# Performance work log

Measured on AMD Instinct MI355X. Metric: run time of the kernel, lower is better.

## Reference

```python
import jax, jax.numpy as jnp
import numpy as np

NUM_BFS_ROUNDS = 32      # fixed-iteration replacement for the set-based BFS (enough hops for N=4096, k=20)
VORONOI_CHUNK = 1024     # must divide B*N


def _knn_self(points, K):
    # brute-force self-KNN over [B,N,3]; idx[...,0] is the query point itself
    sq = jnp.sum(points * points, -1)
    dist = sq[:, :, None] + sq[:, None, :] - 2.0 * jnp.einsum('bnd,bmd->bnm', points, points)
    N = points.shape[1]
    dist = jnp.where(jnp.eye(N, dtype=bool)[None], -1.0, dist)  # force self to rank first
    _, idx = jax.lax.top_k(-dist, K)
    return idx  # [B,N,K] int32


def _gather(x, idx):
    # x [B,N,D], idx [B,N,K] -> [B,N,K,D]
    return jax.vmap(lambda xb, ib: xb[ib])(x, idx)


def _disambiguate(normals, idx):
    # BFS normal-orientation propagation from point 0 (frontier shared across batch, as in the torch code)
    B, N, _ = normals.shape
    frontier0 = jnp.zeros((N,), bool).at[0].set(True)
    visited0 = jnp.zeros((N,), bool)

    def step(carry, _):
        nrm, visited, frontier = carry
        safe_idx = jnp.where(frontier[None, :, None], idx, N)  # non-frontier rows scatter to dummy slot N
        cur = _gather(nrm, idx)                                 # [B,N,K,3]
        sign = jnp.where(jnp.sum(cur * cur[:, :, 0:1, :], -1, keepdims=True) > 0, 1.0, -1.0)
        renew = cur * sign

        def scat(nb, ib, rb):
            pad = jnp.concatenate([nb, jnp.zeros((1, 3), nb.dtype)], 0)
            return pad.at[ib.reshape(-1)].set(rb.reshape(-1, 3))[:N]

        nrm = jax.vmap(scat)(nrm, safe_idx, renew)
        mark = jnp.zeros((N + 1,), bool).at[safe_idx[:, :, 1:].reshape(-1)].set(True)[:N]
        visited = visited | frontier
        frontier = mark & ~visited
        return (nrm, visited, frontier), None

    (normals, _, _), _ = jax.lax.scan(step, (normals, visited0, frontier0), None, length=NUM_BFS_ROUNDS)
    return normals


def _frames_field(points, idx):
    knn_pts = _gather(points, idx)                              # [B,N,K,3]
    centered = knn_pts - knn_pts.mean(-2, keepdims=True)
    # NOTE: divides by (last_dim - 1) == 2, faithfully replicating the original code
    cov = jnp.einsum('bnki,bnkj->bnij', centered, centered) / 2.0
    _, vecs = jnp.linalg.eigh(cov)                              # ascending eigenvalues
    frames = jnp.swapaxes(vecs, -1, -2)                         # rows = eigenvectors; row 0 = normal
    frames = frames.at[:, :, 0, :].set(_disambiguate(frames[:, :, 0, :], idx))
    det = jnp.linalg.det(frames)
    frames = frames.at[:, :, 1, :].set(frames[:, :, 1, :] * det[..., None])
    return frames, knn_pts


def _forward(points, k, local_W):
    B, N = points.shape[:2]
    idx = _knn_self(points, k)
    frames, knn_pts = _frames_field(points, idx)
    dpt = knn_pts - points[:, :, None, :]                       # [B,N,K,3]
    t1 = frames[:, :, 1, :]
    t2 = frames[:, :, 2, :]
    dpt_t = jnp.stack([jnp.sum(dpt * t1[:, :, None, :], -1),
                       jnp.sum(dpt * t2[:, :, None, :], -1)], -1)   # [B,N,K,2]

    # ---- local voronoi area on tangent-plane grid ----
    bmin = dpt_t.min(-2) * 1.1                                  # [B,N,2]
    bmax = dpt_t.max(-2) * 1.1
    maxlen = (bmax - bmin).max(-1)                              # [B,N]
    coord = (dpt_t - bmin[:, :, None, :]) / maxlen[:, :, None, None] * 2.0 - 1.0
    lin = jnp.linspace(-1.0, 1.0, local_W, dtype=points.dtype)
    X, Y = jnp.meshgrid(lin, lin, indexing='ij')
    grid = jnp.stack([X, Y], -1).reshape(-1, 2)                 # [W^2, 2]
    coords_c = jax.lax.stop_gradient(coord).reshape(-1, VORONOI_CHUNK, k, 2)

    def chunk_count(c):  # c [C,k,2] -> count of grid cells whose nearest local point is the center (idx 0)
        d = jnp.sum((grid[None, :, None, :] - c[:, None, :, :]) ** 2, -1)  # [C,W^2,k]
        return jnp.sum(jnp.argmin(d, -1) == 0, -1)

    counts = jax.lax.map(chunk_count, coords_c).reshape(B, N).astype(points.dtype)
    area = counts * maxlen ** 2 / float((local_W - 1) ** 2)     # [B,N]

    # ---- Weingarten fields (non-strict branch) -> gaussian curvature ----
    normals = frames[:, :, 0, :]
    dnrm = _gather(normals, idx) - normals[:, :, None, :]
    dnrm_t = jnp.stack([jnp.sum(dnrm * t1[:, :, None, :], -1),
                        jnp.sum(dnrm * t2[:, :, None, :], -1)], -1)  # [B,N,K,2]
    XXT = jnp.einsum('bnki,bnkj->bnij', dpt_t, dpt_t)
    YXT = jnp.einsum('bnki,bnkj->bnij', dnrm_t, dpt_t)
    Wmat = YXT @ jnp.linalg.inv(XXT + 1e-8 * jnp.eye(2, dtype=points.dtype))
    Wmat = (Wmat + jnp.swapaxes(Wmat, -1, -2)) / 2.0
    gauss = jnp.linalg.det(Wmat)                                # [B,N]

    euler = jnp.sum(gauss * area, -1) / np.pi / 2.0             # [B]
    return euler


def setup_inputs() -> dict:
    key = jax.random.key(0)
    pointscloud = jax.random.normal(key, (2, 4096, 3), dtype=jnp.float32)
    return {"pointscloud": pointscloud, "k": 20, "local_W": 64}


def reference(pointscloud, k, local_W):
    return _forward(pointscloud, k, local_W)
```

## Files before the change

### kernel.cpp

```cpp
#include <hip/hip_runtime.h>
#include <math.h>

#define NPTS  4096
#define BATCH 2
#define KNB   20
#define WGRID 64
#define GCELLS (WGRID * WGRID)
#define NROUNDS 32
#define KBUF  192
#define KQ    16
#define NEDGE (BATCH * NPTS * KNB)
#define NPACK (NEDGE / 16)

__device__ __forceinline__ float knn_dist(const float4 c, const float px,
                                          const float py, const float pz,
                                          const float sqn, const int m,
                                          const int n) {
    const float dot = px * c.x + py * c.y + pz * c.z;
    float dist = (sqn + c.w) - 2.0f * dot;
    if (m == n) dist = -1.0f;
    return dist;
}

__device__ __forceinline__ unsigned long long knn_key(const float dist, const int m) {
    unsigned u = __float_as_uint(dist);
    u = (dist < 0.0f) ? ~u : (u | 0x80000000u);
    return ((unsigned long long)u << 32) | (unsigned)m;
}

__global__ __launch_bounds__(1024, 8) void knn_kernel(const float* __restrict__ pts,
                                                      int* __restrict__ idx) {
    const int tid  = threadIdx.x;
    const int lane = tid & 63;
    const int wid  = tid >> 6;
    const int q    = blockIdx.x * KQ + wid;
    const int b    = q >> 12;
    const int n    = q & (NPTS - 1);
    const float* P = pts + (size_t)b * NPTS * 3;

    __shared__ float4 spts[NPTS];
    __shared__ unsigned short buf[KQ][KBUF];

    for (int i = tid; i < NPTS; i += 1024) {
        const float x = P[i * 3 + 0], y = P[i * 3 + 1], z = P[i * 3 + 2];
        spts[i] = make_float4(x, y, z, x * x + y * y + z * z);
    }
    __syncthreads();

    const float4 me = spts[n];
    const float px = me.x, py = me.y, pz = me.z, sqn = me.w;

    float lmin = 3e38f;
#pragma unroll
    for (int step = 0; step < 64; ++step) {
        const int m = lane + step * 64;
        lmin = fminf(lmin, knn_dist(spts[m], px, py, pz, sqn, m, n));
    }

    float v = lmin;
#pragma unroll
    for (int k = 2; k <= 64; k <<= 1) {
#pragma unroll
        for (int j = k >> 1; j >= 1; j >>= 1) {
            const float o = __shfl_xor(v, j, 64);
            const bool up    = ((lane & k) == 0);
            const bool lower = ((lane & j) == 0);
            v = (lower == up) ? fminf(v, o) : fmaxf(v, o);
        }
    }
    float thr = __shfl(v, 19, 64);
    thr = thr + fabsf(thr) * 1e-4f + 1e-6f;

    unsigned short* wbuf = buf[wid];
    int cnt = 0;
#pragma unroll
    for (int step = 0; step < 64; ++step) {
        const int m = lane + step * 64;
        const float dist = knn_dist(spts[m], px, py, pz, sqn, m, n);
        const bool keep = (dist <= thr);
        const unsigned long long mask = __ballot(keep);
        if (keep) {
            const int pos = cnt + __popcll(mask & ((1ull << lane) - 1ull));
            if (pos < KBUF) wbuf[pos] = (unsigned short)m;
        }
        cnt += __popcll(mask);
    }

    const int M = (cnt < KBUF) ? cnt : KBUF;
    int* op = idx + (size_t)q * KNB;
    const unsigned long long MAXK = ~0ull;
    if (M <= 64) {
        unsigned long long key = MAXK;
        if (lane < M) {
            const int m = (int)wbuf[lane];
            key = knn_key(knn_dist(spts[m], px, py, pz, sqn, m, n), m);
        }
#pragma unroll
        for (int k = 2; k <= 64; k <<= 1) {
#pragma unroll
            for (int j = k >> 1; j >= 1; j >>= 1) {
                const unsigned long long o = __shfl_xor(key, j, 64);
                const bool up    = ((lane & k) == 0);
                const bool lower = ((lane & j) == 0);
                const bool takeMin = (lower == up);
                const unsigned long long mn = key < o ? key : o;
                const unsigned long long mx = key < o ? o : key;
                key = takeMin ? mn : mx;
            }
        }
        if (lane < KNB) op[lane] = (int)(unsigned)(key & 0xffffffffu);
    } else {
        unsigned long long s0 = MAXK, s1 = MAXK, s2 = MAXK;
        if (lane < M) {
            const int m = (int)wbuf[lane];
            s0 = knn_key(knn_dist(spts[m], px, py, pz, sqn, m, n), m);
        }
        if (lane + 64 < M) {
            const int m = (int)wbuf[lane + 64];
            s1 = knn_key(knn_dist(spts[m], px, py, pz, sqn, m, n), m);
        }
        if (lane + 128 < M) {
            const int m = (int)wbuf[lane + 128];
            s2 = knn_key(knn_dist(spts[m], px, py, pz, sqn, m, n), m);
        }
#pragma unroll 1
        for (int r = 0; r < KNB; ++r) {
            unsigned long long kk = s0 < s1 ? s0 : s1;
            kk = kk < s2 ? kk : s2;
#pragma unroll
            for (int off = 32; off; off >>= 1) {
                const unsigned long long ok = __shfl_xor(kk, off, 64);
                kk = ok < kk ? ok : kk;
            }
            if (s0 == kk) s0 = MAXK;
            else if (s1 == kk) s1 = MAXK;
            else if (s2 == kk) s2 = MAXK;
            if (lane == 0) op[r] = (int)(unsigned)(kk & 0xffffffffu);
        }
    }
}

template <int p, int q, int r>
__device__ __forceinline__ void jrot(double A[3][3], double V[3][3]) {
    double apq = A[p][q];
    if (fabs(apq) < 1e-300) return;
    double app = A[p][p], aqq = A[q][q];
    double tau = (aqq - app) / (2.0 * apq);
    double sq  = sqrt(1.0 + tau * tau);
    double t   = (tau >= 0.0) ? (1.0 / (tau + sq)) : (1.0 / (tau - sq));
    double c   = 1.0 / sqrt(1.0 + t * t);
    double s   = t * c;
    A[p][p] = app - t * apq; A[q][q] = aqq + t * apq;
    A[p][q] = 0.0; A[q][p] = 0.0;
    double arp = A[r][p], arq = A[r][q];
    A[r][p] = c * arp - s * arq; A[p][r] = A[r][p];
    A[r][q] = s * arp + c * arq; A[q][r] = A[r][q];
#pragma unroll
    for (int i = 0; i < 3; ++i) {
        double vip = V[i][p], viq = V[i][q];
        V[i][p] = c * vip - s * viq;
        V[i][q] = s * vip + c * viq;
    }
}

__device__ __forceinline__ double selV(const double V[3][3], int i, int c) {
    return c == 0 ? V[i][0] : (c == 1 ? V[i][1] : V[i][2]);
}

__global__ __launch_bounds__(64) void frames_kernel(const float* __restrict__ pts,
                                                    const int* __restrict__ idx,
                                                    float* __restrict__ frames,
                                                    float* __restrict__ normals) {
    const int g = blockIdx.x * 64 + threadIdx.x;
    const int b = g / NPTS;
    const float* P  = pts + (size_t)b * NPTS * 3;
    const int*   ip = idx + (size_t)g * KNB;

    float mx = 0.f, my = 0.f, mz = 0.f;
#pragma unroll
    for (int k = 0; k < KNB; ++k) {
        const int j = ip[k];
        mx += P[j * 3 + 0]; my += P[j * 3 + 1]; mz += P[j * 3 + 2];
    }
    mx /= 20.0f; my /= 20.0f; mz /= 20.0f;

    float c00 = 0.f, c01 = 0.f, c02 = 0.f, c11 = 0.f, c12 = 0.f, c22 = 0.f;
#pragma unroll
    for (int k = 0; k < KNB; ++k) {
        const int j = ip[k];
        const float x = P[j * 3 + 0] - mx;
        const float y = P[j * 3 + 1] - my;
        const float z = P[j * 3 + 2] - mz;
        c00 += x * x; c01 += x * y; c02 += x * z;
        c11 += y * y; c12 += y * z; c22 += z * z;
    }
    c00 *= 0.5f; c01 *= 0.5f; c02 *= 0.5f; c11 *= 0.5f; c12 *= 0.5f; c22 *= 0.5f;

    double A[3][3] = {{c00, c01, c02}, {c01, c11, c12}, {c02, c12, c22}};
    double V[3][3] = {{1, 0, 0}, {0, 1, 0}, {0, 0, 1}};
#pragma unroll
    for (int sw = 0; sw < 10; ++sw) {
        jrot<0, 1, 2>(A, V);
        jrot<0, 2, 1>(A, V);
        jrot<1, 2, 0>(A, V);
    }
    double e0 = A[0][0], e1 = A[1][1], e2 = A[2][2];
    int o0 = 0, o1 = 1, o2 = 2;
    if (e0 > e1) { double t = e0; e0 = e1; e1 = t; int o = o0; o0 = o1; o1 = o; }
    if (e1 > e2) { double t = e1; e1 = e2; e2 = t; int o = o1; o1 = o2; o2 = o; }
    if (e0 > e1) { double t = e0; e0 = e1; e1 = t; int o = o0; o0 = o1; o1 = o; }

    float* F = frames + (size_t)g * 9;
    F[0] = (float)selV(V, 0, o0); F[1] = (float)selV(V, 1, o0); F[2] = (float)selV(V, 2, o0);
    F[3] = (float)selV(V, 0, o1); F[4] = (float)selV(V, 1, o1); F[5] = (float)selV(V, 2, o1);
    F[6] = (float)selV(V, 0, o2); F[7] = (float)selV(V, 1, o2); F[8] = (float)selV(V, 2, o2);
    normals[(size_t)g * 3 + 0] = F[0];
    normals[(size_t)g * 3 + 1] = F[1];
    normals[(size_t)g * 3 + 2] = F[2];
}

__global__ __launch_bounds__(256) void edgesign_kernel(const int* __restrict__ idx,
                                                       const float* __restrict__ normals,
                                                       unsigned* __restrict__ dsgnp,
                                                       unsigned short* __restrict__ idx16) {
    const int e = blockIdx.x * 256 + threadIdx.x;
    const int lane = threadIdx.x & 63;
    const int b = e / (NPTS * KNB);
    const int r = e - b * NPTS * KNB;
    const int n = r / KNB;
    const int j = idx[e];
    idx16[e] = (unsigned short)j;
    const float* NB = normals + (size_t)b * NPTS * 3;
    const float d = __fadd_rn(__fadd_rn(__fmul_rn(NB[j * 3 + 0], NB[n * 3 + 0]),
                                        __fmul_rn(NB[j * 3 + 1], NB[n * 3 + 1])),
                              __fmul_rn(NB[j * 3 + 2], NB[n * 3 + 2]));
    const unsigned long long m0 = __ballot(d == 0.0f);
    const unsigned long long m1 = __ballot(d > 0.0f);
    if (lane < 4) {
        unsigned x = (unsigned)(m0 >> (lane * 16)) & 0xFFFFu;
        unsigned y = (unsigned)(m1 >> (lane * 16)) & 0xFFFFu;
        x = (x | (x << 8)) & 0x00FF00FFu; x = (x | (x << 4)) & 0x0F0F0F0Fu;
        x = (x | (x << 2)) & 0x33333333u; x = (x | (x << 1)) & 0x55555555u;
        y = (y | (y << 8)) & 0x00FF00FFu; y = (y | (y << 4)) & 0x0F0F0F0Fu;
        y = (y | (y << 2)) & 0x33333333u; y = (y | (y << 1)) & 0x55555555u;
        dsgnp[((e - lane) >> 4) + lane] = x | (y << 1);
    }
}

__global__ __launch_bounds__(1024) void bfs_kernel(const unsigned short* __restrict__ idx16,
                                                   const unsigned* __restrict__ dsgnp,
                                                   float* __restrict__ nrm) {
    const int tid = threadIdx.x;
    const int lane = tid & 63;
    __shared__ int winner[BATCH * NPTS];
    __shared__ signed char sgbuf[2][BATCH * NPTS];
    __shared__ unsigned dsp[NPACK];
    __shared__ unsigned short list[NPTS];
    __shared__ unsigned char EL[NPTS];
    __shared__ int cntsh;

    {
        unsigned wacc = 0;
        const uint4* ip4 = (const uint4*)idx16;
#pragma unroll 4
        for (int i = tid; i < (NEDGE * 2) / 16; i += 1024) {
            const uint4 v = ip4[i];
            wacc ^= v.x ^ v.y ^ v.z ^ v.w;
        }
        asm volatile("" :: "v"(wacc));
    }

    for (int j = tid; j < NPTS; j += 1024) {
        winner[j] = 0; winner[NPTS + j] = 0;
        sgbuf[0][j] = 1; sgbuf[0][NPTS + j] = 1;
        EL[j] = 0;
    }
    for (int i = tid; i < NPACK; i += 1024) dsp[i] = dsgnp[i];
    if (tid == 0) { cntsh = 1; list[0] = 0; EL[0] = 1; }
    __syncthreads();

    int cur = 0;
    int rstart = 0, rend = 1;
    for (int round = 0; round < NROUNDS; ++round) {
        const int tag = (round + 1) << 17;
        const int items = (rend - rstart) * BATCH;
        for (int base = 0; base < items; base += 4096) {
            unsigned pr[4][KNB / 2];
            int tflat[4], wbase[4];
            bool ok[4];
#pragma unroll
            for (int s = 0; s < 4; ++s) {
                const int w = base + s * 1024 + tid;
                ok[s] = (w < items);
                if (ok[s]) {
                    const int i = w >> 1, b = w & 1;
                    const int n0 = (int)list[rstart + i];
                    tflat[s] = tag + n0 * KNB;
                    wbase[s] = b * NPTS;
                    const unsigned* rp =
                        (const unsigned*)(idx16 + ((size_t)b * NPTS + n0) * KNB);
#pragma unroll
                    for (int u = 0; u < KNB / 2; ++u) pr[s][u] = rp[u];
                }
            }
#pragma unroll
            for (int s = 0; s < 4; ++s) {
                if (ok[s]) {
#pragma unroll
                    for (int u = 0; u < KNB / 2; ++u) {
                        const int j0 = (int)(pr[s][u] & 0xffffu);
                        const int j1 = (int)(pr[s][u] >> 16);
                        atomicMax(&winner[wbase[s] + j0], tflat[s] + 2 * u);
                        atomicMax(&winner[wbase[s] + j1], tflat[s] + 2 * u + 1);
                    }
                }
            }
        }
        __syncthreads();
        const signed char* sgOld = sgbuf[cur];
        signed char* sgNew = sgbuf[cur ^ 1];
#pragma unroll
        for (int u = 0; u < 4; ++u) {
            const int j = tid + u * 1024;
            bool marked = false;
#pragma unroll
            for (int b = 0; b < BATCH; ++b) {
                const int bj = b * NPTS + j;
                const int w = winner[bj];
                signed char s = sgOld[bj];
                if (w >= tag) {
                    const int flat = w - tag;
                    const int nsrc = flat / KNB;
                    const int wi = b * (NPTS * KNB) + flat;
                    const int d = (int)((dsp[wi >> 4] >> ((wi & 15) << 1)) & 3u) - 1;
                    const signed char sn = sgOld[b * NPTS + nsrc];
                    s = d ? (signed char)(d * sn) : (signed char)(-s);
                    if (flat % KNB != 0) marked = true;
                }
                sgNew[bj] = s;
            }
            const bool f = marked && !EL[j];
            if (f) EL[j] = 1;
            const unsigned long long mask = __ballot(f);
            if (mask) {
                const int lead = (int)(__ffsll((long long)mask) - 1);
                int basep = 0;
                if (lane == lead) basep = atomicAdd(&cntsh, (int)__popcll(mask));
                basep = __shfl(basep, lead, 64);
                if (f) list[basep + (int)__popcll(mask & ((1ull << lane) - 1ull))] =
                           (unsigned short)j;
            }
        }
        __syncthreads();
        cur ^= 1;
        rstart = rend;
        rend = cntsh;
        if (rstart == rend) break;
    }
    const signed char* sgF = sgbuf[cur];
    for (int i = tid; i < BATCH * NPTS * 3; i += 1024) {
        if (sgF[i / 3] < 0) nrm[i] = -nrm[i];
    }
}

__global__ __launch_bounds__(256) void geom_kernel(const float* __restrict__ pts,
                                                   const int* __restrict__ idx,
                                                   const float* __restrict__ frames,
                                                   const float* __restrict__ nrm,
                                                   double* __restrict__ pervals) {
    const int lane = threadIdx.x & 63;
    const int q = blockIdx.x * 4 + (threadIdx.x >> 6);
    const int b = q >> 12, n = q & (NPTS - 1);
    const float* P  = pts + (size_t)b * NPTS * 3;
    const float* NR = nrm + (size_t)b * NPTS * 3;
    const float* F  = frames + (size_t)q * 9;

    const float v0x = NR[n * 3 + 0], v0y = NR[n * 3 + 1], v0z = NR[n * 3 + 2];
    const float v1x = F[3], v1y = F[4], v1z = F[5];
    const float v2x = F[6], v2y = F[7], v2z = F[8];
    const float det = v0x * (v1y * v2z - v1z * v2y)
                    - v0y * (v1x * v2z - v1z * v2x)
                    + v0z * (v1x * v2y - v1y * v2x);
    const float t1x = v1x * det, t1y = v1y * det, t1z = v1z * det;
    const float t2x = v2x, t2y = v2y, t2z = v2z;

    const bool isk = lane < KNB;
    float ptx = 0.f, pty = 0.f, qtx = 0.f, qty = 0.f;
    if (isk) {
        const int j = idx[(size_t)q * KNB + lane];
        const float dx = P[j * 3 + 0] - P[n * 3 + 0];
        const float dy = P[j * 3 + 1] - P[n * 3 + 1];
        const float dz = P[j * 3 + 2] - P[n * 3 + 2];
        ptx = dx * t1x + dy * t1y + dz * t1z;
        pty = dx * t2x + dy * t2y + dz * t2z;
        const float ex = NR[j * 3 + 0] - v0x;
        const float ey = NR[j * 3 + 1] - v0y;
        const float ez = NR[j * 3 + 2] - v0z;
        qtx = ex * t1x + ey * t1y + ez * t1z;
        qty = ex * t2x + ey * t2y + ez * t2z;
    }

    float mnx = isk ? ptx :  3e38f, mny = isk ? pty :  3e38f;
    float mxx = isk ? ptx : -3e38f, mxy = isk ? pty : -3e38f;
#pragma unroll
    for (int off = 32; off; off >>= 1) {
        mnx = fminf(mnx, __shfl_xor(mnx, off, 64));
        mny = fminf(mny, __shfl_xor(mny, off, 64));
        mxx = fmaxf(mxx, __shfl_xor(mxx, off, 64));
        mxy = fmaxf(mxy, __shfl_xor(mxy, off, 64));
    }
    mnx *= 1.1f; mny *= 1.1f; mxx *= 1.1f; mxy *= 1.1f;
    const float ml = fmaxf(mxx - mnx, mxy - mny);

    const float cx = (ptx - mnx) / ml * 2.0f - 1.0f;
    const float cy = (pty - mny) / ml * 2.0f - 1.0f;
    const float c0x = __shfl(cx, 0, 64), c0y = __shfl(cy, 0, 64);

    const float ax = 2.0f * (cx - c0x);
    const float ay = 2.0f * (cy - c0y);
    const float bbk = cx * cx + cy * cy - (c0x * c0x + c0y * c0y);
    const float inva = (ay != 0.0f) ? (1.0f / ay) : 0.0f;

    const float gx = (float)(-1.0 + (2.0 * (double)lane) / 63.0);
    float lo = -3e38f, hi = 3e38f;
    bool feas = true;
#pragma unroll
    for (int k = 1; k < KNB; ++k) {
        const float axk = __shfl(ax, k, 64);
        const float ayk = __shfl(ay, k, 64);
        const float bk  = __shfl(bbk, k, 64);
        const float ik  = __shfl(inva, k, 64);
        const float rk  = bk - gx * axk;
        const float t   = rk * ik;
        if (ayk > 0.0f)      hi = fminf(hi, t);
        else if (ayk < 0.0f) lo = fmaxf(lo, t);
        else                 feas = feas && (rk >= 0.0f);
    }
    int cnt = 0;
    if (feas) {
        const float hif = fminf((hi + 1.0f) * 31.5f, 63.0f);
        const float lof = fmaxf((lo + 1.0f) * 31.5f, 0.0f);
        const int jhi = (int)floorf(hif);
        const int jlo = (int)ceilf(lof);
        cnt = jhi - jlo + 1;
        if (cnt < 0) cnt = 0;
    }
#pragma unroll
    for (int off = 32; off; off >>= 1) cnt += __shfl_xor(cnt, off, 64);
    const float area = (float)cnt * ml * ml / 3969.0f;

    double xx00 = 0, xx01 = 0, xx11 = 0, yx00 = 0, yx01 = 0, yx10 = 0, yx11 = 0;
    if (isk) {
        const double px = ptx, py = pty, qx2 = qtx, qy2 = qty;
        xx00 = px * px; xx01 = px * py; xx11 = py * py;
        yx00 = qx2 * px; yx01 = qx2 * py; yx10 = qy2 * px; yx11 = qy2 * py;
    }
#pragma unroll
    for (int off = 32; off; off >>= 1) {
        xx00 += __shfl_xor(xx00, off, 64);
        xx01 += __shfl_xor(xx01, off, 64);
        xx11 += __shfl_xor(xx11, off, 64);
        yx00 += __shfl_xor(yx00, off, 64);
        yx01 += __shfl_xor(yx01, off, 64);
        yx10 += __shfl_xor(yx10, off, 64);
        yx11 += __shfl_xor(yx11, off, 64);
    }
    if (lane == 0) {
        const double m00 = xx00 + 1e-8, m01 = xx01, m11 = xx11 + 1e-8;
        const double dm = m00 * m11 - m01 * m01;
        const double i00 = m11 / dm, i01 = -m01 / dm, i11 = m00 / dm;
        const double w00 = yx00 * i00 + yx01 * i01;
        const double w01 = yx00 * i01 + yx01 * i11;
        const double w10 = yx10 * i00 + yx11 * i01;
        const double w11 = yx10 * i01 + yx11 * i11;
        const double off2 = 0.5 * (w01 + w10);
        const double gauss = w00 * w11 - off2 * off2;
        pervals[q] = gauss * (double)area;
    }
}

__global__ __launch_bounds__(256) void reduce_kernel(const double* __restrict__ pervals,
                                                     float* __restrict__ out) {
    const int b = blockIdx.x, tid = threadIdx.x;
    __shared__ double sm[256];
    double s = 0.0;
    for (int i = tid; i < NPTS; i += 256) s += pervals[(size_t)b * NPTS + i];
    sm[tid] = s;
    __syncthreads();
    for (int st = 128; st > 0; st >>= 1) {
        if (tid < st) sm[tid] += sm[tid + st];
        __syncthreads();
    }
    if (tid == 0) out[b] = (float)(sm[0] / 3.14159265358979323846 / 2.0);
}

extern "C" void kernel_launch(void* const* d_in, const int* in_sizes, int n_in,
                              void* d_out, int out_size, void* d_ws, size_t ws_size,
                              hipStream_t stream) {
    (void)in_sizes; (void)n_in; (void)out_size; (void)ws_size;
    const float* pts = (const float*)d_in[0];
    char* ws = (char*)d_ws;

    size_t off = 0;
    double* pervals = (double*)(ws + off); off += (size_t)BATCH * NPTS * sizeof(double);
    int*    idx     = (int*)(ws + off);    off += (size_t)BATCH * NPTS * KNB * sizeof(int);
    float*  frames  = (float*)(ws + off);  off += (size_t)BATCH * NPTS * 9 * sizeof(float);
    float*  normals = (float*)(ws + off);  off += (size_t)BATCH * NPTS * 3 * sizeof(float);
    unsigned short* idx16 = (unsigned short*)(ws + off);
    off += (size_t)BATCH * NPTS * KNB * sizeof(unsigned short);
    unsigned* dsgnp = (unsigned*)(ws + off);
    off += (size_t)NPACK * sizeof(unsigned);

    knn_kernel<<<BATCH * NPTS / KQ, 1024, 0, stream>>>(pts, idx);
    frames_kernel<<<BATCH * NPTS / 64, 64, 0, stream>>>(pts, idx, frames, normals);
    edgesign_kernel<<<BATCH * NPTS * KNB / 256, 256, 0, stream>>>(idx, normals, dsgnp, idx16);
    bfs_kernel<<<1, 1024, 0, stream>>>(idx16, dsgnp, normals);
    geom_kernel<<<BATCH * NPTS / 4, 256, 0, stream>>>(pts, idx, frames, normals, pervals);
    reduce_kernel<<<BATCH, 256, 0, stream>>>(pervals, (float*)d_out);
}
```

Before: 100.5 us.

## Process four KNN queries per wavefront to reuse shared point loads

Each wavefront in the KNN kernel now handles four query points instead of one. Every candidate float4 read from shared memory is reused across all four distance computations, and the bitonic threshold and sort steps are interleaved across queries. Blocks shrink to 512 threads with 32 queries each, so fewer blocks each stage the point cloud into LDS. The change also drops a prefetch/warm-up read of idx16 at the start of the BFS kernel. In exchange, register pressure rises and occupancy may fall.

```diff
diff --git a/kernel.cpp b/kernel.cpp
--- a/kernel.cpp
+++ b/kernel.cpp
@@ -8,7 +8,9 @@
 #define GCELLS (WGRID * WGRID)
 #define NROUNDS 32
 #define KBUF  192
-#define KQ    16
+#define KQW   4
+#define WPB   8
+#define QPB   (KQW * WPB)
 #define NEDGE (BATCH * NPTS * KNB)
 #define NPACK (NEDGE / 16)
 
@@ -28,114 +30,150 @@
     return ((unsigned long long)u << 32) | (unsigned)m;
 }
 
-__global__ __launch_bounds__(1024, 8) void knn_kernel(const float* __restrict__ pts,
-                                                      int* __restrict__ idx) {
+__global__ __launch_bounds__(512, 4) void knn_kernel(const float* __restrict__ pts,
+                                                     int* __restrict__ idx) {
     const int tid  = threadIdx.x;
     const int lane = tid & 63;
     const int wid  = tid >> 6;
-    const int q    = blockIdx.x * KQ + wid;
-    const int b    = q >> 12;
-    const int n    = q & (NPTS - 1);
+    const int qbase = blockIdx.x * QPB + wid * KQW;
+    const int b    = qbase >> 12;
     const float* P = pts + (size_t)b * NPTS * 3;
 
     __shared__ float4 spts[NPTS];
-    __shared__ unsigned short buf[KQ][KBUF];
-
-    for (int i = tid; i < NPTS; i += 1024) {
+    __shared__ unsigned short buf[QPB][KBUF];
+
+    for (int i = tid; i < NPTS; i += 512) {
         const float x = P[i * 3 + 0], y = P[i * 3 + 1], z = P[i * 3 + 2];
         spts[i] = make_float4(x, y, z, x * x + y * y + z * z);
     }
     __syncthreads();
 
-    const float4 me = spts[n];
-    const float px = me.x, py = me.y, pz = me.z, sqn = me.w;
-
-    float lmin = 3e38f;
-#pragma unroll
+    int nq[KQW];
+    float px[KQW], py[KQW], pz[KQW], sqn[KQW];
+#pragma unroll
+    for (int qq = 0; qq < KQW; ++qq) {
+        nq[qq] = (qbase & (NPTS - 1)) + qq;
+        const float4 me = spts[nq[qq]];
+        px[qq] = me.x; py[qq] = me.y; pz[qq] = me.z; sqn[qq] = me.w;
+    }
+
+    float v[KQW];
+#pragma unroll
+    for (int qq = 0; qq < KQW; ++qq) v[qq] = 3e38f;
+#pragma unroll 4
     for (int step = 0; step < 64; ++step) {
         const int m = lane + step * 64;
-        lmin = fminf(lmin, knn_dist(spts[m], px, py, pz, sqn, m, n));
-    }
-
-    float v = lmin;
+        const float4 c = spts[m];
+#pragma unroll
+        for (int qq = 0; qq < KQW; ++qq)
+            v[qq] = fminf(v[qq], knn_dist(c, px[qq], py[qq], pz[qq], sqn[qq], m, nq[qq]));
+    }
+
 #pragma unroll
     for (int k = 2; k <= 64; k <<= 1) {
 #pragma unroll
         for (int j = k >> 1; j >= 1; j >>= 1) {
-            const float o = __shfl_xor(v, j, 64);
             const bool up    = ((lane & k) == 0);
             const bool lower = ((lane & j) == 0);
-            v = (lower == up) ? fminf(v, o) : fmaxf(v, o);
-        }
-    }
-    float thr = __shfl(v, 19, 64);
-    thr = thr + fabsf(thr) * 1e-4f + 1e-6f;
-
-    unsigned short* wbuf = buf[wid];
-    int cnt = 0;
-#pragma unroll
+            const bool takeMin = (lower == up);
+#pragma unroll
+            for (int qq = 0; qq < KQW; ++qq) {
+                const float o = __shfl_xor(v[qq], j, 64);
+                v[qq] = takeMin ? fminf(v[qq], o) : fmaxf(v[qq], o);
+            }
+        }
+    }
+    float thr[KQW];
+#pragma unroll
+    for (int qq = 0; qq < KQW; ++qq) {
+        float t = __shfl(v[qq], 19, 64);
+        thr[qq] = t + fabsf(t) * 1e-4f + 1e-6f;
+    }
+
+    int cnt[KQW];
+#pragma unroll
+    for (int qq = 0; qq < KQW; ++qq) cnt[qq] = 0;
+#pragma unroll 2
     for (int step = 0; step < 64; ++step) {
         const int m = lane + step * 64;
-        const float dist = knn_dist(spts[m], px, py, pz, sqn, m, n);
-        const bool keep = (dist <= thr);
-        const unsigned long long mask = __ballot(keep);
-        if (keep) {
-            const int pos = cnt + __popcll(mask & ((1ull << lane) - 1ull));
-            if (pos < KBUF) wbuf[pos] = (unsigned short)m;
-        }
-        cnt += __popcll(mask);
-    }
-
-    const int M = (cnt < KBUF) ? cnt : KBUF;
-    int* op = idx + (size_t)q * KNB;
+        const float4 c = spts[m];
+#pragma unroll
+        for (int qq = 0; qq < KQW; ++qq) {
+            const float dist = knn_dist(c, px[qq], py[qq], pz[qq], sqn[qq], m, nq[qq]);
+            const bool keep = (dist <= thr[qq]);
+            const unsigned long long mask = __ballot(keep);
+            if (keep) {
+                const int pos = cnt[qq] + __popcll(mask & ((1ull << lane) - 1ull));
+                if (pos < KBUF) buf[wid * KQW + qq][pos] = (unsigned short)m;
+            }
+            cnt[qq] += __popcll(mask);
+        }
+    }
+
     const unsigned long long MAXK = ~0ull;
-    if (M <= 64) {
-        unsigned long long key = MAXK;
-        if (lane < M) {
-            const int m = (int)wbuf[lane];
-            key = knn_key(knn_dist(spts[m], px, py, pz, sqn, m, n), m);
-        }
-#pragma unroll
-        for (int k = 2; k <= 64; k <<= 1) {
-#pragma unroll
-            for (int j = k >> 1; j >= 1; j >>= 1) {
-                const unsigned long long o = __shfl_xor(key, j, 64);
-                const bool up    = ((lane & k) == 0);
-                const bool lower = ((lane & j) == 0);
-                const bool takeMin = (lower == up);
-                const unsigned long long mn = key < o ? key : o;
-                const unsigned long long mx = key < o ? o : key;
-                key = takeMin ? mn : mx;
-            }
-        }
-        if (lane < KNB) op[lane] = (int)(unsigned)(key & 0xffffffffu);
-    } else {
-        unsigned long long s0 = MAXK, s1 = MAXK, s2 = MAXK;
-        if (lane < M) {
-            const int m = (int)wbuf[lane];
-            s0 = knn_key(knn_dist(spts[m], px, py, pz, sqn, m, n), m);
-        }
-        if (lane + 64 < M) {
-            const int m = (int)wbuf[lane + 64];
-            s1 = knn_key(knn_dist(spts[m], px, py, pz, sqn, m, n), m);
-        }
-        if (lane + 128 < M) {
-            const int m = (int)wbuf[lane + 128];
-            s2 = knn_key(knn_dist(spts[m], px, py, pz, sqn, m, n), m);
-        }
+    unsigned long long key[KQW];
+    int M[KQW];
+    bool big[KQW];
+#pragma unroll
+    for (int qq = 0; qq < KQW; ++qq) {
+        M[qq] = (cnt[qq] < KBUF) ? cnt[qq] : KBUF;
+        big[qq] = (M[qq] > 64);
+        key[qq] = MAXK;
+        if (!big[qq] && lane < M[qq]) {
+            const int m = (int)buf[wid * KQW + qq][lane];
+            key[qq] = knn_key(knn_dist(spts[m], px[qq], py[qq], pz[qq], sqn[qq],
+                                       m, nq[qq]), m);
+        }
+    }
+#pragma unroll
+    for (int k = 2; k <= 64; k <<= 1) {
+#pragma unroll
+        for (int j = k >> 1; j >= 1; j >>= 1) {
+            const bool up    = ((lane & k) == 0);
+            const bool lower = ((lane & j) == 0);
+            const bool takeMin = (lower == up);
+#pragma unroll
+            for (int qq = 0; qq < KQW; ++qq) {
+                const unsigned long long o = __shfl_xor(key[qq], j, 64);
+                const unsigned long long mn = key[qq] < o ? key[qq] : o;
+                const unsigned long long mx = key[qq] < o ? o : key[qq];
+                key[qq] = takeMin ? mn : mx;
+            }
+        }
+    }
+#pragma unroll
+    for (int qq = 0; qq < KQW; ++qq) {
+        int* op = idx + (size_t)(qbase + qq) * KNB;
+        if (!big[qq]) {
+            if (lane < KNB) op[lane] = (int)(unsigned)(key[qq] & 0xffffffffu);
+        } else {
+            unsigned long long s0 = MAXK, s1 = MAXK, s2 = MAXK;
+            if (lane < M[qq]) {
+                const int m = (int)buf[wid * KQW + qq][lane];
+                s0 = knn_key(knn_dist(spts[m], px[qq], py[qq], pz[qq], sqn[qq], m, nq[qq]), m);
+            }
+            if (lane + 64 < M[qq]) {
+                const int m = (int)buf[wid * KQW + qq][lane + 64];
+                s1 = knn_key(knn_dist(spts[m], px[qq], py[qq], pz[qq], sqn[qq], m, nq[qq]), m);
+            }
+            if (lane + 128 < M[qq]) {
+                const int m = (int)buf[wid * KQW + qq][lane + 128];
+                s2 = knn_key(knn_dist(spts[m], px[qq], py[qq], pz[qq], sqn[qq], m, nq[qq]), m);
+            }
 #pragma unroll 1
-        for (int r = 0; r < KNB; ++r) {
-            unsigned long long kk = s0 < s1 ? s0 : s1;
-            kk = kk < s2 ? kk : s2;
-#pragma unroll
-            for (int off = 32; off; off >>= 1) {
-                const unsigned long long ok = __shfl_xor(kk, off, 64);
-                kk = ok < kk ? ok : kk;
-            }
-            if (s0 == kk) s0 = MAXK;
-            else if (s1 == kk) s1 = MAXK;
-            else if (s2 == kk) s2 = MAXK;
-            if (lane == 0) op[r] = (int)(unsigned)(kk & 0xffffffffu);
+            for (int r = 0; r < KNB; ++r) {
+                unsigned long long kk = s0 < s1 ? s0 : s1;
+                kk = kk < s2 ? kk : s2;
+#pragma unroll
+                for (int off = 32; off; off >>= 1) {
+                    const unsigned long long ok = __shfl_xor(kk, off, 64);
+                    kk = ok < kk ? ok : kk;
+                }
+                if (s0 == kk) s0 = MAXK;
+                else if (s1 == kk) s1 = MAXK;
+                else if (s2 == kk) s2 = MAXK;
+                if (lane == 0) op[r] = (int)(unsigned)(kk & 0xffffffffu);
+            }
         }
     }
 }
@@ -259,17 +297,6 @@
     __shared__ unsigned char EL[NPTS];
     __shared__ int cntsh;
 
-    {
-        unsigned wacc = 0;
-        const uint4* ip4 = (const uint4*)idx16;
-#pragma unroll 4
-        for (int i = tid; i < (NEDGE * 2) / 16; i += 1024) {
-            const uint4 v = ip4[i];
-            wacc ^= v.x ^ v.y ^ v.z ^ v.w;
-        }
-        asm volatile("" :: "v"(wacc));
-    }
-
     for (int j = tid; j < NPTS; j += 1024) {
         winner[j] = 0; winner[NPTS + j] = 0;
         sgbuf[0][j] = 1; sgbuf[0][NPTS + j] = 1;
@@ -511,7 +538,7 @@
     unsigned* dsgnp = (unsigned*)(ws + off);
     off += (size_t)NPACK * sizeof(unsigned);
 
-    knn_kernel<<<BATCH * NPTS / KQ, 1024, 0, stream>>>(pts, idx);
+    knn_kernel<<<BATCH * NPTS / QPB, 512, 0, stream>>>(pts, idx);
     frames_kernel<<<BATCH * NPTS / 64, 64, 0, stream>>>(pts, idx, frames, normals);
     edgesign_kernel<<<BATCH * NPTS * KNB / 256, 256, 0, stream>>>(idx, normals, dsgnp, idx16);
     bfs_kernel<<<1, 1024, 0, stream>>>(idx16, dsgnp, normals);
```

Result: slower. 109.2 us (+8.6%).

## Skip untouched 64-point groups in BFS sign update using dirty flags

Applied to the files above, without the earlier changes.

Replaces the double-buffered sign array with a single in-place array plus a frontier-sign snapshot, so only signs that change need to be written each round. Per-round dirty flags mark 64-point groups that received any scatter, and the update pass skips clean groups wholesale. It also removes the warm-up pass that read the whole idx16 array into registers. The cost is extra shared-memory stores for the dirty flags in the atomic loop and more intricate ordering between the snapshot and the in-place update.

```diff
diff --git a/kernel.cpp b/kernel.cpp
--- a/kernel.cpp
+++ b/kernel.cpp
@@ -253,36 +253,28 @@
     const int tid = threadIdx.x;
     const int lane = tid & 63;
     __shared__ int winner[BATCH * NPTS];
-    __shared__ signed char sgbuf[2][BATCH * NPTS];
+    __shared__ signed char sg[BATCH * NPTS];
+    __shared__ signed char fsg[BATCH * NPTS];
     __shared__ unsigned dsp[NPACK];
     __shared__ unsigned short list[NPTS];
     __shared__ unsigned char EL[NPTS];
+    __shared__ unsigned char dirtyG[2][64];
     __shared__ int cntsh;
-
-    {
-        unsigned wacc = 0;
-        const uint4* ip4 = (const uint4*)idx16;
-#pragma unroll 4
-        for (int i = tid; i < (NEDGE * 2) / 16; i += 1024) {
-            const uint4 v = ip4[i];
-            wacc ^= v.x ^ v.y ^ v.z ^ v.w;
-        }
-        asm volatile("" :: "v"(wacc));
-    }
 
     for (int j = tid; j < NPTS; j += 1024) {
         winner[j] = 0; winner[NPTS + j] = 0;
-        sgbuf[0][j] = 1; sgbuf[0][NPTS + j] = 1;
+        sg[j] = 1; sg[NPTS + j] = 1;
         EL[j] = 0;
     }
     for (int i = tid; i < NPACK; i += 1024) dsp[i] = dsgnp[i];
+    if (tid < 128) dirtyG[tid >> 6][tid & 63] = 0;
     if (tid == 0) { cntsh = 1; list[0] = 0; EL[0] = 1; }
     __syncthreads();
 
-    int cur = 0;
     int rstart = 0, rend = 1;
     for (int round = 0; round < NROUNDS; ++round) {
         const int tag = (round + 1) << 17;
+        const int par = round & 1;
         const int items = (rend - rstart) * BATCH;
         for (int base = 0; base < items; base += 4096) {
             unsigned pr[4][KNB / 2];
@@ -297,6 +289,7 @@
                     const int n0 = (int)list[rstart + i];
                     tflat[s] = tag + n0 * KNB;
                     wbase[s] = b * NPTS;
+                    fsg[b * NPTS + n0] = sg[b * NPTS + n0];
                     const unsigned* rp =
                         (const unsigned*)(idx16 + ((size_t)b * NPTS + n0) * KNB);
 #pragma unroll
@@ -310,6 +303,8 @@
                     for (int u = 0; u < KNB / 2; ++u) {
                         const int j0 = (int)(pr[s][u] & 0xffffu);
                         const int j1 = (int)(pr[s][u] >> 16);
+                        dirtyG[par][j0 >> 6] = 1;
+                        dirtyG[par][j1 >> 6] = 1;
                         atomicMax(&winner[wbase[s] + j0], tflat[s] + 2 * u);
                         atomicMax(&winner[wbase[s] + j1], tflat[s] + 2 * u + 1);
                     }
@@ -317,27 +312,25 @@
             }
         }
         __syncthreads();
-        const signed char* sgOld = sgbuf[cur];
-        signed char* sgNew = sgbuf[cur ^ 1];
 #pragma unroll
         for (int u = 0; u < 4; ++u) {
             const int j = tid + u * 1024;
+            const int g = j >> 6;
+            if (!dirtyG[par][g]) continue;
             bool marked = false;
 #pragma unroll
             for (int b = 0; b < BATCH; ++b) {
                 const int bj = b * NPTS + j;
                 const int w = winner[bj];
-                signed char s = sgOld[bj];
                 if (w >= tag) {
                     const int flat = w - tag;
                     const int nsrc = flat / KNB;
                     const int wi = b * (NPTS * KNB) + flat;
                     const int d = (int)((dsp[wi >> 4] >> ((wi & 15) << 1)) & 3u) - 1;
-                    const signed char sn = sgOld[b * NPTS + nsrc];
-                    s = d ? (signed char)(d * sn) : (signed char)(-s);
+                    const signed char sn = fsg[b * NPTS + nsrc];
+                    sg[bj] = d ? (signed char)(d * sn) : (signed char)(-sg[bj]);
                     if (flat % KNB != 0) marked = true;
                 }
-                sgNew[bj] = s;
             }
             const bool f = marked && !EL[j];
             if (f) EL[j] = 1;
@@ -351,15 +344,14 @@
                            (unsigned short)j;
             }
         }
+        if (tid < 64) dirtyG[par ^ 1][tid] = 0;
         __syncthreads();
-        cur ^= 1;
         rstart = rend;
         rend = cntsh;
         if (rstart == rend) break;
     }
-    const signed char* sgF = sgbuf[cur];
     for (int i = tid; i < BATCH * NPTS * 3; i += 1024) {
-        if (sgF[i / 3] < 0) nrm[i] = -nrm[i];
+        if (sg[i / 3] < 0) nrm[i] = -nrm[i];
     }
 }
 
```

Result: slower. 106.7 us (+6.1%).
